# Kernel tuning notes

Hardware: AMD Instinct MI355X
Metric: run time of the kernel (lower is better)

## Reference

```python
import jax, jax.numpy as jnp
import numpy as np

N = 10000       # num_nodes
E = 1000        # num_hyperedges
STEPS = 30      # horizon


def setup_inputs() -> dict:
    key = jax.random.key(0)
    k1, k2 = jax.random.split(key, 2)
    infected0 = jax.random.uniform(k1, (N,)) < 0.01
    x = jnp.stack([(~infected0).astype(jnp.float32),
                   infected0.astype(jnp.float32),
                   jnp.zeros((N,), jnp.float32)], axis=1)
    H = (jax.random.uniform(k2, (STEPS - 1, E, N)) < 0.001).astype(jnp.float32)
    beta = jnp.full((N,), 0.01, jnp.float32)
    gamma = jnp.full((N,), 0.038, jnp.float32)
    return {"x": x, "H": H, "beta": beta, "gamma": gamma, "steps": STEPS}


def _simulate(x, H, beta, gamma):
    n = x.shape[0]
    key0 = jax.random.key(42)

    def step(carry, H_t):
        p_prev, s_prev, key = carry
        key, k1, k2 = jax.random.split(key, 3)
        infected = s_prev[:, 1]
        # hypergraph Laplacian step: H_t.T @ (H_t @ infected)
        new_cases = beta * (H_t.T @ (H_t @ infected))
        new_rec = gamma * infected
        p = jnp.stack([p_prev[:, 0] - new_cases,
                       p_prev[:, 1] + new_cases - new_rec,
                       p_prev[:, 2] + new_rec], axis=1)
        p = jnp.clip(p, 0.0, 1.0)
        # per-node stochastic SIR state transitions (vectorized)
        u1 = jax.random.uniform(k1, (n,))
        u2 = jax.random.uniform(k2, (n,))
        was_S = s_prev[:, 0] == 1
        was_I = s_prev[:, 1] == 1
        s_to_I = was_S & (u1 < p[:, 1])
        i_event = was_I & (u1 < p[:, 2])
        i_to_R = i_event & (u2 < 0.5)
        i_to_S = i_event & ~(u2 < 0.5)
        new_S = (was_S & ~s_to_I) | i_to_S
        new_I = s_to_I | (was_I & ~i_event)
        new_R = (~was_S & ~was_I) | i_to_R
        s = jnp.stack([new_S, new_I, new_R], axis=1).astype(x.dtype)
        return (p, s, key), (p, s)

    (_, _, _), (p_seq, s_seq) = jax.lax.scan(step, (x, x, key0), H)
    pathogen = jnp.concatenate([x[None], p_seq], axis=0)    # (steps, N, 3)
    state = jnp.concatenate([x[None], s_seq], axis=0)       # (steps, N, 3)
    return pathogen, state


def reference(x, H, beta, gamma, steps):
    # steps == H.shape[0] + 1 by construction
    return _simulate(x, H, beta, gamma)
```

## Files before the change

### kernel.cpp

```cpp
#include <hip/hip_runtime.h>
#include <stdint.h>

constexpr int NN = 10000;
constexpr int EE = 1000;
constexpr int TT = 30;
constexpr int TS = TT - 1;
constexpr int ROW = NN * 3;
constexpr int S_OFF = TT * ROW;
constexpr int CAP_E = 48;
constexpr int SIMT = 1024;
constexpr int NPT  = 10;

__host__ __device__ inline void tf2x32(uint32_t k0, uint32_t k1,
                                       uint32_t x0, uint32_t x1,
                                       uint32_t &o0, uint32_t &o1) {
  uint32_t ks2 = k0 ^ k1 ^ 0x1BD11BDAu;
  x0 += k0; x1 += k1;
#define TFR(r) do { x0 += x1; x1 = (x1 << (r)) | (x1 >> (32 - (r))); x1 ^= x0; } while (0)
  TFR(13); TFR(15); TFR(26); TFR(6);
  x0 += k1;  x1 += ks2 + 1u;
  TFR(17); TFR(29); TFR(16); TFR(24);
  x0 += ks2; x1 += k0 + 2u;
  TFR(13); TFR(15); TFR(26); TFR(6);
  x0 += k0;  x1 += k1 + 3u;
  TFR(17); TFR(29); TFR(16); TFR(24);
  x0 += k1;  x1 += ks2 + 4u;
  TFR(13); TFR(15); TFR(26); TFR(6);
  x0 += ks2; x1 += k0 + 5u;
#undef TFR
  o0 = x0; o1 = x1;
}

__device__ inline float bits_to_uniform(uint32_t bits) {
  float f = __uint_as_float((bits >> 9) | 0x3F800000u) - 1.0f;
  return f < 0.f ? 0.f : f;
}

struct StepKeys { uint32_t k1a[TS], k1b[TS], k2a[TS], k2b[TS]; };

__global__ void k_init(const float* __restrict__ x, float* __restrict__ out) {
  int i = blockIdx.x * blockDim.x + threadIdx.x;
  if (i < ROW) { out[i] = x[i]; out[S_OFF + i] = x[i]; }
}

__global__ void k_rand(float* __restrict__ u1, float* __restrict__ u2, StepKeys keys) {
  int t = blockIdx.y;
  int n = blockIdx.x * blockDim.x + threadIdx.x;
  if (n >= NN) return;
  uint32_t a, b;
  tf2x32(keys.k1a[t], keys.k1b[t], 0u, (uint32_t)n, a, b);
  u1[t * NN + n] = bits_to_uniform(a ^ b);
  tf2x32(keys.k2a[t], keys.k2b[t], 0u, (uint32_t)n, a, b);
  u2[t * NN + n] = bits_to_uniform(a ^ b);
}

__global__ void k_scan(const float* __restrict__ H, int* __restrict__ edge_cnt,
                       uint16_t* __restrict__ edge_nodes) {
  const int row = blockIdx.x;
  const int t = row / EE;
  const int e = row - t * EE;
  __shared__ int cnt;
  __shared__ uint16_t list[CAP_E];
  if (threadIdx.x == 0) cnt = 0;
  __syncthreads();
  const float4* hrow = reinterpret_cast<const float4*>(H + (size_t)row * NN);
  for (int i = threadIdx.x; i < NN / 4; i += blockDim.x) {
    float4 v = hrow[i];
    int b4 = i * 4;
    if (v.x != 0.f) { int p = atomicAdd(&cnt, 1); if (p < CAP_E) list[p] = (uint16_t)(b4 + 0); }
    if (v.y != 0.f) { int p = atomicAdd(&cnt, 1); if (p < CAP_E) list[p] = (uint16_t)(b4 + 1); }
    if (v.z != 0.f) { int p = atomicAdd(&cnt, 1); if (p < CAP_E) list[p] = (uint16_t)(b4 + 2); }
    if (v.w != 0.f) { int p = atomicAdd(&cnt, 1); if (p < CAP_E) list[p] = (uint16_t)(b4 + 3); }
  }
  __syncthreads();
  int c = cnt < CAP_E ? cnt : CAP_E;
  if (threadIdx.x == 0) edge_cnt[row] = c;
  if ((int)threadIdx.x < c)
    edge_nodes[((size_t)t * CAP_E + threadIdx.x) * EE + e] = list[threadIdx.x];
}

__global__ __launch_bounds__(SIMT, 4)
void k_sim(float* __restrict__ out, const float* __restrict__ x,
           const int* __restrict__ edge_cnt, const uint16_t* __restrict__ edge_nodes,
           const float* __restrict__ u1, const float* __restrict__ u2,
           const float* __restrict__ beta, const float* __restrict__ gamma_) {
  __shared__ uint8_t s_st[NN];
  __shared__ int nv[NN];
  const int tid = threadIdx.x;

  float p0[NPT], p1[NPT], p2[NPT], bet[NPT], gam[NPT];
#pragma unroll
  for (int k = 0; k < NPT; ++k) {
    int n = tid + k * SIMT;
    if (n < NN) {
      float x0 = x[n * 3 + 0], x1 = x[n * 3 + 1], x2 = x[n * 3 + 2];
      p0[k] = x0; p1[k] = x1; p2[k] = x2;
      s_st[n] = (x1 == 1.f) ? 1 : ((x0 == 1.f) ? 0 : 2);
      bet[k] = beta[n]; gam[k] = gamma_[n];
    }
  }
  __syncthreads();

  for (int t = 0; t < TS; ++t) {
#pragma unroll
    for (int k = 0; k < NPT; ++k) { int n = tid + k * SIMT; if (n < NN) nv[n] = 0; }
    __syncthreads();

    if (tid < EE) {
      int row = t * EE + tid;
      int ec = edge_cnt[row];
      const uint16_t* base = edge_nodes + (size_t)t * CAP_E * EE + tid;
      int s = 0;
      for (int m = 0; m < ec; ++m) s += (s_st[base[(size_t)m * EE]] == 1) ? 1 : 0;
      for (int m = 0; m < ec; ++m) atomicAdd(&nv[base[(size_t)m * EE]], s);
    }
    __syncthreads();

    float* po = out + (size_t)(t + 1) * ROW;
    float* so = out + S_OFF + (size_t)(t + 1) * ROW;
    const float* u1t = u1 + (size_t)t * NN;
    const float* u2t = u2 + (size_t)t * NN;
#pragma unroll
    for (int k = 0; k < NPT; ++k) {
      int n = tid + k * SIMT;
      if (n < NN) {
        int st = s_st[n];
        float s1 = (st == 1) ? 1.f : 0.f;
        float new_cases = __fmul_rn(bet[k], (float)nv[n]);
        float new_rec   = __fmul_rn(gam[k], s1);
        float q0 = fminf(1.f, fmaxf(0.f, __fsub_rn(p0[k], new_cases)));
        float q1 = fminf(1.f, fmaxf(0.f, __fsub_rn(__fadd_rn(p1[k], new_cases), new_rec)));
        float q2 = fminf(1.f, fmaxf(0.f, __fadd_rn(p2[k], new_rec)));
        p0[k] = q0; p1[k] = q1; p2[k] = q2;

        float uu1 = u1t[n], uu2 = u2t[n];
        bool was_S  = (st == 0);
        bool was_I  = (st == 1);
        bool s_to_I = was_S && (uu1 < q1);
        bool i_event = was_I && (uu1 < q2);
        bool u2lt   = (uu2 < 0.5f);
        bool i_to_R = i_event && u2lt;
        bool i_to_S = i_event && !u2lt;
        bool new_S = (was_S && !s_to_I) || i_to_S;
        bool new_I = s_to_I || (was_I && !i_event);
        bool new_R = (!was_S && !was_I) || i_to_R;

        po[n * 3 + 0] = q0; po[n * 3 + 1] = q1; po[n * 3 + 2] = q2;
        so[n * 3 + 0] = new_S ? 1.f : 0.f;
        so[n * 3 + 1] = new_I ? 1.f : 0.f;
        so[n * 3 + 2] = new_R ? 1.f : 0.f;
        s_st[n] = new_I ? 1 : (new_S ? 0 : 2);
      }
    }
    __syncthreads();
  }
}

extern "C" void kernel_launch(void* const* d_in, const int* in_sizes, int n_in,
                              void* d_out, int out_size, void* d_ws, size_t ws_size,
                              hipStream_t stream) {
  const float* x      = (const float*)d_in[0];
  const float* H      = (const float*)d_in[1];
  const float* beta   = (const float*)d_in[2];
  const float* gamma_ = (const float*)d_in[3];
  float* out = (float*)d_out;

  StepKeys keys;
  uint32_t key0 = 0u, key1 = 42u;
  for (int t = 0; t < TS; ++t) {
    uint32_t a0, b0, a1, b1, a2, b2;
    tf2x32(key0, key1, 0u, 0u, a0, b0);
    tf2x32(key0, key1, 0u, 1u, a1, b1);
    tf2x32(key0, key1, 0u, 2u, a2, b2);
    keys.k1a[t] = a1; keys.k1b[t] = b1; keys.k2a[t] = a2; keys.k2b[t] = b2;
    key0 = a0; key1 = b0;
  }

  size_t off = 0;
  auto take = [&](size_t bytes) { size_t o = off; off += (bytes + 255) & ~(size_t)255; return o; };
  size_t o_ec = take((size_t)TS * EE * sizeof(int));
  size_t o_en = take((size_t)TS * EE * CAP_E * sizeof(uint16_t));
  size_t o_u1 = take((size_t)TS * NN * sizeof(float));
  size_t o_u2 = take((size_t)TS * NN * sizeof(float));

  int*      edge_cnt   = (int*)((char*)d_ws + o_ec);
  uint16_t* edge_nodes = (uint16_t*)((char*)d_ws + o_en);
  float*    u1         = (float*)((char*)d_ws + o_u1);
  float*    u2         = (float*)((char*)d_ws + o_u2);

  k_init<<<(ROW + 255) / 256, 256, 0, stream>>>(x, out);
  k_rand<<<dim3((NN + 255) / 256, TS), 256, 0, stream>>>(u1, u2, keys);
  k_scan<<<TS * EE, 256, 0, stream>>>(H, edge_cnt, edge_nodes);
  k_sim<<<1, SIMT, 0, stream>>>(out, x, edge_cnt, edge_nodes, u1, u2, beta, gamma_);
}
```

Before: 1.798 ms.

## Move float output writes out of single-block sim into parallel expand kernel

The single-workgroup simulation kernel now writes only compact per-step uint8 states and uint16 neighbour counts to workspace, instead of six strided floats per node per step. A new grid-wide k_expand kernel replays the cheap probability recurrence from those compact arrays and writes the full pathogen and state outputs in parallel. This moves most of the global-store traffic off the serial one-block critical path, at the cost of an extra launch and recomputation. The uint16 truncation of neighbour counts assumes counts stay below 65536.

```diff
diff --git a/kernel.cpp b/kernel.cpp
--- a/kernel.cpp
+++ b/kernel.cpp
@@ -38,11 +38,6 @@
 
 struct StepKeys { uint32_t k1a[TS], k1b[TS], k2a[TS], k2b[TS]; };
 
-__global__ void k_init(const float* __restrict__ x, float* __restrict__ out) {
-  int i = blockIdx.x * blockDim.x + threadIdx.x;
-  if (i < ROW) { out[i] = x[i]; out[S_OFF + i] = x[i]; }
-}
-
 __global__ void k_rand(float* __restrict__ u1, float* __restrict__ u2, StepKeys keys) {
   int t = blockIdx.y;
   int n = blockIdx.x * blockDim.x + threadIdx.x;
@@ -80,10 +75,11 @@
 }
 
 __global__ __launch_bounds__(SIMT, 4)
-void k_sim(float* __restrict__ out, const float* __restrict__ x,
+void k_sim(const float* __restrict__ x,
            const int* __restrict__ edge_cnt, const uint16_t* __restrict__ edge_nodes,
            const float* __restrict__ u1, const float* __restrict__ u2,
-           const float* __restrict__ beta, const float* __restrict__ gamma_) {
+           const float* __restrict__ beta, const float* __restrict__ gamma_,
+           uint16_t* __restrict__ nvA, uint8_t* __restrict__ stA) {
   __shared__ uint8_t s_st[NN];
   __shared__ int nv[NN];
   const int tid = threadIdx.x;
@@ -93,9 +89,11 @@
   for (int k = 0; k < NPT; ++k) {
     int n = tid + k * SIMT;
     if (n < NN) {
-      float x0 = x[n * 3 + 0], x1 = x[n * 3 + 1], x2 = x[n * 3 + 2];
-      p0[k] = x0; p1[k] = x1; p2[k] = x2;
-      s_st[n] = (x1 == 1.f) ? 1 : ((x0 == 1.f) ? 0 : 2);
+      float x0 = x[n * 3 + 0], x1 = x[n * 3 + 1];
+      p0[k] = x0; p1[k] = x1; p2[k] = x[n * 3 + 2];
+      uint8_t c = (x1 == 1.f) ? 1 : ((x0 == 1.f) ? 0 : 2);
+      s_st[n] = c;
+      stA[n] = c;
       bet[k] = beta[n]; gam[k] = gamma_[n];
     }
   }
@@ -116,17 +114,18 @@
     }
     __syncthreads();
 
-    float* po = out + (size_t)(t + 1) * ROW;
-    float* so = out + S_OFF + (size_t)(t + 1) * ROW;
     const float* u1t = u1 + (size_t)t * NN;
     const float* u2t = u2 + (size_t)t * NN;
+    uint16_t* nvO = nvA + (size_t)t * NN;
+    uint8_t*  stO = stA + (size_t)(t + 1) * NN;
 #pragma unroll
     for (int k = 0; k < NPT; ++k) {
       int n = tid + k * SIMT;
       if (n < NN) {
         int st = s_st[n];
+        int v = nv[n];
         float s1 = (st == 1) ? 1.f : 0.f;
-        float new_cases = __fmul_rn(bet[k], (float)nv[n]);
+        float new_cases = __fmul_rn(bet[k], (float)v);
         float new_rec   = __fmul_rn(gam[k], s1);
         float q0 = fminf(1.f, fmaxf(0.f, __fsub_rn(p0[k], new_cases)));
         float q1 = fminf(1.f, fmaxf(0.f, __fsub_rn(__fadd_rn(p1[k], new_cases), new_rec)));
@@ -139,20 +138,43 @@
         bool s_to_I = was_S && (uu1 < q1);
         bool i_event = was_I && (uu1 < q2);
         bool u2lt   = (uu2 < 0.5f);
-        bool i_to_R = i_event && u2lt;
         bool i_to_S = i_event && !u2lt;
         bool new_S = (was_S && !s_to_I) || i_to_S;
         bool new_I = s_to_I || (was_I && !i_event);
-        bool new_R = (!was_S && !was_I) || i_to_R;
-
-        po[n * 3 + 0] = q0; po[n * 3 + 1] = q1; po[n * 3 + 2] = q2;
-        so[n * 3 + 0] = new_S ? 1.f : 0.f;
-        so[n * 3 + 1] = new_I ? 1.f : 0.f;
-        so[n * 3 + 2] = new_R ? 1.f : 0.f;
-        s_st[n] = new_I ? 1 : (new_S ? 0 : 2);
+        uint8_t c = new_I ? 1 : (new_S ? 0 : 2);
+        s_st[n] = c;
+        stO[n] = c;
+        nvO[n] = (uint16_t)v;
       }
     }
     __syncthreads();
+  }
+}
+
+__global__ void k_expand(float* __restrict__ out, const float* __restrict__ x,
+                         const uint16_t* __restrict__ nvA, const uint8_t* __restrict__ stA,
+                         const float* __restrict__ beta, const float* __restrict__ gamma_) {
+  int n = blockIdx.x * blockDim.x + threadIdx.x;
+  if (n >= NN) return;
+  float p0 = x[n * 3 + 0], p1 = x[n * 3 + 1], p2 = x[n * 3 + 2];
+  float bet = beta[n], gam = gamma_[n];
+  out[n * 3 + 0] = p0; out[n * 3 + 1] = p1; out[n * 3 + 2] = p2;
+  out[S_OFF + n * 3 + 0] = p0; out[S_OFF + n * 3 + 1] = p1; out[S_OFF + n * 3 + 2] = p2;
+  for (int t = 0; t < TS; ++t) {
+    int st = stA[(size_t)t * NN + n];
+    float s1 = (st == 1) ? 1.f : 0.f;
+    float new_cases = __fmul_rn(bet, (float)nvA[(size_t)t * NN + n]);
+    float new_rec   = __fmul_rn(gam, s1);
+    p0 = fminf(1.f, fmaxf(0.f, __fsub_rn(p0, new_cases)));
+    p1 = fminf(1.f, fmaxf(0.f, __fsub_rn(__fadd_rn(p1, new_cases), new_rec)));
+    p2 = fminf(1.f, fmaxf(0.f, __fadd_rn(p2, new_rec)));
+    float* po = out + (size_t)(t + 1) * ROW;
+    float* so = out + S_OFF + (size_t)(t + 1) * ROW;
+    po[n * 3 + 0] = p0; po[n * 3 + 1] = p1; po[n * 3 + 2] = p2;
+    int sn = stA[(size_t)(t + 1) * NN + n];
+    so[n * 3 + 0] = (sn == 0) ? 1.f : 0.f;
+    so[n * 3 + 1] = (sn == 1) ? 1.f : 0.f;
+    so[n * 3 + 2] = (sn == 2) ? 1.f : 0.f;
   }
 }
 
@@ -182,14 +204,18 @@
   size_t o_en = take((size_t)TS * EE * CAP_E * sizeof(uint16_t));
   size_t o_u1 = take((size_t)TS * NN * sizeof(float));
   size_t o_u2 = take((size_t)TS * NN * sizeof(float));
+  size_t o_nv = take((size_t)TS * NN * sizeof(uint16_t));
+  size_t o_st = take((size_t)TT * NN * sizeof(uint8_t));
 
   int*      edge_cnt   = (int*)((char*)d_ws + o_ec);
   uint16_t* edge_nodes = (uint16_t*)((char*)d_ws + o_en);
   float*    u1         = (float*)((char*)d_ws + o_u1);
   float*    u2         = (float*)((char*)d_ws + o_u2);
-
-  k_init<<<(ROW + 255) / 256, 256, 0, stream>>>(x, out);
+  uint16_t* nvA        = (uint16_t*)((char*)d_ws + o_nv);
+  uint8_t*  stA        = (uint8_t*)((char*)d_ws + o_st);
+
   k_rand<<<dim3((NN + 255) / 256, TS), 256, 0, stream>>>(u1, u2, keys);
   k_scan<<<TS * EE, 256, 0, stream>>>(H, edge_cnt, edge_nodes);
-  k_sim<<<1, SIMT, 0, stream>>>(out, x, edge_cnt, edge_nodes, u1, u2, beta, gamma_);
-}
+  k_sim<<<1, SIMT, 0, stream>>>(x, edge_cnt, edge_nodes, u1, u2, beta, gamma_, nvA, stA);
+  k_expand<<<(NN + 255) / 256, 256, 0, stream>>>(out, x, nvA, stA, beta, gamma_);
+}
```

Measured after the change: 1.880 ms. +4.5%, slower.

## Fuse scan and simulation into one kernel with per-step producer/consumer flags

Applied to the files above, without the earlier changes.

Merges the H-row compaction kernel and the single-block simulation kernel into one launch. Block 0 runs the sequential simulation and spins on a per-timestep counter, while the other blocks compact H rows and signal completion with release atomics, so the serial simulation can overlap the bandwidth-bound scan. It also folds the init copy into the sim block, packs edge node indices two per 32-bit word, skips scatter when an edge has no infected nodes, prefetches the random numbers into registers, and drops one barrier per step. The design relies on block 0 being scheduled before the producer blocks and staying resident; otherwise it could deadlock. Scan blocks now use 1024 threads, which may lower scan efficiency.

```diff
diff --git a/kernel.cpp b/kernel.cpp
--- a/kernel.cpp
+++ b/kernel.cpp
@@ -8,6 +8,7 @@
 constexpr int ROW = NN * 3;
 constexpr int S_OFF = TT * ROW;
 constexpr int CAP_E = 48;
+constexpr int WPR = CAP_E / 2;
 constexpr int SIMT = 1024;
 constexpr int NPT  = 10;
 
@@ -38,14 +39,11 @@
 
 struct StepKeys { uint32_t k1a[TS], k1b[TS], k2a[TS], k2b[TS]; };
 
-__global__ void k_init(const float* __restrict__ x, float* __restrict__ out) {
-  int i = blockIdx.x * blockDim.x + threadIdx.x;
-  if (i < ROW) { out[i] = x[i]; out[S_OFF + i] = x[i]; }
-}
-
-__global__ void k_rand(float* __restrict__ u1, float* __restrict__ u2, StepKeys keys) {
+__global__ void k_rand(float* __restrict__ u1, float* __restrict__ u2,
+                       unsigned* __restrict__ cnt, StepKeys keys) {
   int t = blockIdx.y;
   int n = blockIdx.x * blockDim.x + threadIdx.x;
+  if (blockIdx.x == 0 && blockIdx.y == 0 && threadIdx.x < TS) cnt[threadIdx.x] = 0u;
   if (n >= NN) return;
   uint32_t a, b;
   tf2x32(keys.k1a[t], keys.k1b[t], 0u, (uint32_t)n, a, b);
@@ -54,39 +52,50 @@
   u2[t * NN + n] = bits_to_uniform(a ^ b);
 }
 
-__global__ void k_scan(const float* __restrict__ H, int* __restrict__ edge_cnt,
-                       uint16_t* __restrict__ edge_nodes) {
-  const int row = blockIdx.x;
-  const int t = row / EE;
-  const int e = row - t * EE;
-  __shared__ int cnt;
-  __shared__ uint16_t list[CAP_E];
-  if (threadIdx.x == 0) cnt = 0;
-  __syncthreads();
-  const float4* hrow = reinterpret_cast<const float4*>(H + (size_t)row * NN);
-  for (int i = threadIdx.x; i < NN / 4; i += blockDim.x) {
-    float4 v = hrow[i];
-    int b4 = i * 4;
-    if (v.x != 0.f) { int p = atomicAdd(&cnt, 1); if (p < CAP_E) list[p] = (uint16_t)(b4 + 0); }
-    if (v.y != 0.f) { int p = atomicAdd(&cnt, 1); if (p < CAP_E) list[p] = (uint16_t)(b4 + 1); }
-    if (v.z != 0.f) { int p = atomicAdd(&cnt, 1); if (p < CAP_E) list[p] = (uint16_t)(b4 + 2); }
-    if (v.w != 0.f) { int p = atomicAdd(&cnt, 1); if (p < CAP_E) list[p] = (uint16_t)(b4 + 3); }
-  }
-  __syncthreads();
-  int c = cnt < CAP_E ? cnt : CAP_E;
-  if (threadIdx.x == 0) edge_cnt[row] = c;
-  if ((int)threadIdx.x < c)
-    edge_nodes[((size_t)t * CAP_E + threadIdx.x) * EE + e] = list[threadIdx.x];
-}
-
-__global__ __launch_bounds__(SIMT, 4)
-void k_sim(float* __restrict__ out, const float* __restrict__ x,
-           const int* __restrict__ edge_cnt, const uint16_t* __restrict__ edge_nodes,
-           const float* __restrict__ u1, const float* __restrict__ u2,
-           const float* __restrict__ beta, const float* __restrict__ gamma_) {
+__global__ __launch_bounds__(SIMT, 1)
+void k_fused(const float* __restrict__ H,
+             int* __restrict__ edge_cnt, uint32_t* __restrict__ edge_words,
+             unsigned* __restrict__ cnt,
+             const float* __restrict__ x,
+             const float* __restrict__ u1, const float* __restrict__ u2,
+             const float* __restrict__ beta, const float* __restrict__ gamma_,
+             float* __restrict__ out) {
+  const int tid = threadIdx.x;
+
+  if (blockIdx.x > 0) {
+    const int row = blockIdx.x - 1;
+    const int t = row / EE;
+    const int e = row - t * EE;
+    __shared__ int scnt;
+    __shared__ uint16_t list[CAP_E];
+    if (tid == 0) scnt = 0;
+    __syncthreads();
+    const float4* hrow = reinterpret_cast<const float4*>(H + (size_t)row * NN);
+    for (int i = tid; i < NN / 4; i += SIMT) {
+      float4 v = hrow[i];
+      int b4 = i * 4;
+      if (v.x != 0.f) { int p = atomicAdd(&scnt, 1); if (p < CAP_E) list[p] = (uint16_t)(b4 + 0); }
+      if (v.y != 0.f) { int p = atomicAdd(&scnt, 1); if (p < CAP_E) list[p] = (uint16_t)(b4 + 1); }
+      if (v.z != 0.f) { int p = atomicAdd(&scnt, 1); if (p < CAP_E) list[p] = (uint16_t)(b4 + 2); }
+      if (v.w != 0.f) { int p = atomicAdd(&scnt, 1); if (p < CAP_E) list[p] = (uint16_t)(b4 + 3); }
+    }
+    __syncthreads();
+    int c = scnt < CAP_E ? scnt : CAP_E;
+    if (tid == 0) edge_cnt[row] = c;
+    int words = (c + 1) >> 1;
+    if (tid < words) {
+      uint32_t lo = list[2 * tid];
+      uint32_t hi = (2 * tid + 1 < c) ? (uint32_t)list[2 * tid + 1] : 0xFFFFu;
+      edge_words[((size_t)t * WPR + tid) * EE + e] = lo | (hi << 16);
+    }
+    __syncthreads();
+    if (tid == 0)
+      __hip_atomic_fetch_add(&cnt[t], 1u, __ATOMIC_RELEASE, __HIP_MEMORY_SCOPE_AGENT);
+    return;
+  }
+
   __shared__ uint8_t s_st[NN];
   __shared__ int nv[NN];
-  const int tid = threadIdx.x;
 
   float p0[NPT], p1[NPT], p2[NPT], bet[NPT], gam[NPT];
 #pragma unroll
@@ -96,49 +105,77 @@
       float x0 = x[n * 3 + 0], x1 = x[n * 3 + 1], x2 = x[n * 3 + 2];
       p0[k] = x0; p1[k] = x1; p2[k] = x2;
       s_st[n] = (x1 == 1.f) ? 1 : ((x0 == 1.f) ? 0 : 2);
+      nv[n] = 0;
       bet[k] = beta[n]; gam[k] = gamma_[n];
+      out[n * 3 + 0] = x0; out[n * 3 + 1] = x1; out[n * 3 + 2] = x2;
+      out[S_OFF + n * 3 + 0] = x0; out[S_OFF + n * 3 + 1] = x1; out[S_OFF + n * 3 + 2] = x2;
     }
   }
   __syncthreads();
 
   for (int t = 0; t < TS; ++t) {
+    float u1r[NPT], u2r[NPT];
 #pragma unroll
-    for (int k = 0; k < NPT; ++k) { int n = tid + k * SIMT; if (n < NN) nv[n] = 0; }
+    for (int k = 0; k < NPT; ++k) {
+      int n = tid + k * SIMT;
+      if (n < NN) { u1r[k] = u1[(size_t)t * NN + n]; u2r[k] = u2[(size_t)t * NN + n]; }
+    }
+    if (tid == 0) {
+      while (__hip_atomic_load(&cnt[t], __ATOMIC_ACQUIRE, __HIP_MEMORY_SCOPE_AGENT)
+             < (unsigned)EE) {
+        __builtin_amdgcn_s_sleep(16);
+      }
+    }
     __syncthreads();
 
     if (tid < EE) {
-      int row = t * EE + tid;
-      int ec = edge_cnt[row];
-      const uint16_t* base = edge_nodes + (size_t)t * CAP_E * EE + tid;
+      int ec = __hip_atomic_load(&edge_cnt[t * EE + tid], __ATOMIC_RELAXED,
+                                 __HIP_MEMORY_SCOPE_AGENT);
+      if (ec > CAP_E) ec = CAP_E;
+      int words = (ec + 1) >> 1;
+      const uint32_t* wb = edge_words + (size_t)t * WPR * EE + tid;
       int s = 0;
-      for (int m = 0; m < ec; ++m) s += (s_st[base[(size_t)m * EE]] == 1) ? 1 : 0;
-      for (int m = 0; m < ec; ++m) atomicAdd(&nv[base[(size_t)m * EE]], s);
+      for (int mw = 0; mw < words; ++mw) {
+        uint32_t w = __hip_atomic_load(&wb[(size_t)mw * EE], __ATOMIC_RELAXED,
+                                       __HIP_MEMORY_SCOPE_AGENT);
+        s += (s_st[w & 0xFFFFu] == 1) ? 1 : 0;
+        uint32_t hi = w >> 16;
+        if (hi != 0xFFFFu) s += (s_st[hi] == 1) ? 1 : 0;
+      }
+      if (s > 0) {
+        for (int mw = 0; mw < words; ++mw) {
+          uint32_t w = __hip_atomic_load(&wb[(size_t)mw * EE], __ATOMIC_RELAXED,
+                                         __HIP_MEMORY_SCOPE_AGENT);
+          atomicAdd(&nv[w & 0xFFFFu], s);
+          uint32_t hi = w >> 16;
+          if (hi != 0xFFFFu) atomicAdd(&nv[(int)hi], s);
+        }
+      }
     }
     __syncthreads();
 
     float* po = out + (size_t)(t + 1) * ROW;
     float* so = out + S_OFF + (size_t)(t + 1) * ROW;
-    const float* u1t = u1 + (size_t)t * NN;
-    const float* u2t = u2 + (size_t)t * NN;
 #pragma unroll
     for (int k = 0; k < NPT; ++k) {
       int n = tid + k * SIMT;
       if (n < NN) {
         int st = s_st[n];
+        int v = nv[n];
+        nv[n] = 0;
         float s1 = (st == 1) ? 1.f : 0.f;
-        float new_cases = __fmul_rn(bet[k], (float)nv[n]);
+        float new_cases = __fmul_rn(bet[k], (float)v);
         float new_rec   = __fmul_rn(gam[k], s1);
         float q0 = fminf(1.f, fmaxf(0.f, __fsub_rn(p0[k], new_cases)));
         float q1 = fminf(1.f, fmaxf(0.f, __fsub_rn(__fadd_rn(p1[k], new_cases), new_rec)));
         float q2 = fminf(1.f, fmaxf(0.f, __fadd_rn(p2[k], new_rec)));
         p0[k] = q0; p1[k] = q1; p2[k] = q2;
 
-        float uu1 = u1t[n], uu2 = u2t[n];
         bool was_S  = (st == 0);
         bool was_I  = (st == 1);
-        bool s_to_I = was_S && (uu1 < q1);
-        bool i_event = was_I && (uu1 < q2);
-        bool u2lt   = (uu2 < 0.5f);
+        bool s_to_I = was_S && (u1r[k] < q1);
+        bool i_event = was_I && (u1r[k] < q2);
+        bool u2lt   = (u2r[k] < 0.5f);
         bool i_to_R = i_event && u2lt;
         bool i_to_S = i_event && !u2lt;
         bool new_S = (was_S && !s_to_I) || i_to_S;
@@ -152,7 +189,6 @@
         s_st[n] = new_I ? 1 : (new_S ? 0 : 2);
       }
     }
-    __syncthreads();
   }
 }
 
@@ -179,17 +215,18 @@
   size_t off = 0;
   auto take = [&](size_t bytes) { size_t o = off; off += (bytes + 255) & ~(size_t)255; return o; };
   size_t o_ec = take((size_t)TS * EE * sizeof(int));
-  size_t o_en = take((size_t)TS * EE * CAP_E * sizeof(uint16_t));
+  size_t o_ew = take((size_t)TS * WPR * EE * sizeof(uint32_t));
   size_t o_u1 = take((size_t)TS * NN * sizeof(float));
   size_t o_u2 = take((size_t)TS * NN * sizeof(float));
+  size_t o_ct = take((size_t)TS * sizeof(unsigned));
 
   int*      edge_cnt   = (int*)((char*)d_ws + o_ec);
-  uint16_t* edge_nodes = (uint16_t*)((char*)d_ws + o_en);
+  uint32_t* edge_words = (uint32_t*)((char*)d_ws + o_ew);
   float*    u1         = (float*)((char*)d_ws + o_u1);
   float*    u2         = (float*)((char*)d_ws + o_u2);
-
-  k_init<<<(ROW + 255) / 256, 256, 0, stream>>>(x, out);
-  k_rand<<<dim3((NN + 255) / 256, TS), 256, 0, stream>>>(u1, u2, keys);
-  k_scan<<<TS * EE, 256, 0, stream>>>(H, edge_cnt, edge_nodes);
-  k_sim<<<1, SIMT, 0, stream>>>(out, x, edge_cnt, edge_nodes, u1, u2, beta, gamma_);
-}
+  unsigned* cnt        = (unsigned*)((char*)d_ws + o_ct);
+
+  k_rand<<<dim3((NN + 255) / 256, TS), 256, 0, stream>>>(u1, u2, cnt, keys);
+  k_fused<<<1 + TS * EE, SIMT, 0, stream>>>(H, edge_cnt, edge_words, cnt,
+                                            x, u1, u2, beta, gamma_, out);
+}
```

Result: slower. 2.122 ms (+18.0%).

## Pack edge node lists, prefetch, cut barriers and fold init into sim kernel

Applied to the files above, without the earlier changes.

Edge node indices are packed two per 32-bit word with sentinel padding, and the first eight words are prefetched unconditionally so the gather loop is unrolled. The per-step clearing of the count array moves into the update loop, which removes one barrier per step. The remaining barriers become a raw LDS waitcnt plus s_barrier. Random uniforms are loaded before the edge phase, edges with no infected nodes skip their atomics, and the init kernel is merged into the sim kernel. The cost is a more complex scan output layout, and the hand-written barrier relies on no global memory ordering being needed across it.

```diff
diff --git a/kernel.cpp b/kernel.cpp
--- a/kernel.cpp
+++ b/kernel.cpp
@@ -8,6 +8,8 @@
 constexpr int ROW = NN * 3;
 constexpr int S_OFF = TT * ROW;
 constexpr int CAP_E = 48;
+constexpr int WPR = CAP_E / 2;
+constexpr int PREW = 8;
 constexpr int SIMT = 1024;
 constexpr int NPT  = 10;
 
@@ -38,9 +40,8 @@
 
 struct StepKeys { uint32_t k1a[TS], k1b[TS], k2a[TS], k2b[TS]; };
 
-__global__ void k_init(const float* __restrict__ x, float* __restrict__ out) {
-  int i = blockIdx.x * blockDim.x + threadIdx.x;
-  if (i < ROW) { out[i] = x[i]; out[S_OFF + i] = x[i]; }
+__device__ inline void bar_lds() {
+  asm volatile("s_waitcnt lgkmcnt(0)\n\ts_barrier" ::: "memory");
 }
 
 __global__ void k_rand(float* __restrict__ u1, float* __restrict__ u2, StepKeys keys) {
@@ -55,7 +56,7 @@
 }
 
 __global__ void k_scan(const float* __restrict__ H, int* __restrict__ edge_cnt,
-                       uint16_t* __restrict__ edge_nodes) {
+                       uint32_t* __restrict__ edge_words) {
   const int row = blockIdx.x;
   const int t = row / EE;
   const int e = row - t * EE;
@@ -75,13 +76,19 @@
   __syncthreads();
   int c = cnt < CAP_E ? cnt : CAP_E;
   if (threadIdx.x == 0) edge_cnt[row] = c;
-  if ((int)threadIdx.x < c)
-    edge_nodes[((size_t)t * CAP_E + threadIdx.x) * EE + e] = list[threadIdx.x];
+  int words = (c + 1) >> 1;
+  int wmax = words > PREW ? words : PREW;
+  if ((int)threadIdx.x < wmax) {
+    int j = threadIdx.x;
+    uint32_t lo = (2 * j     < c) ? (uint32_t)list[2 * j]     : 0xFFFFu;
+    uint32_t hi = (2 * j + 1 < c) ? (uint32_t)list[2 * j + 1] : 0xFFFFu;
+    edge_words[((size_t)t * WPR + j) * EE + e] = lo | (hi << 16);
+  }
 }
 
 __global__ __launch_bounds__(SIMT, 4)
 void k_sim(float* __restrict__ out, const float* __restrict__ x,
-           const int* __restrict__ edge_cnt, const uint16_t* __restrict__ edge_nodes,
+           const int* __restrict__ edge_cnt, const uint32_t* __restrict__ edge_words,
            const float* __restrict__ u1, const float* __restrict__ u2,
            const float* __restrict__ beta, const float* __restrict__ gamma_) {
   __shared__ uint8_t s_st[NN];
@@ -96,49 +103,81 @@
       float x0 = x[n * 3 + 0], x1 = x[n * 3 + 1], x2 = x[n * 3 + 2];
       p0[k] = x0; p1[k] = x1; p2[k] = x2;
       s_st[n] = (x1 == 1.f) ? 1 : ((x0 == 1.f) ? 0 : 2);
+      nv[n] = 0;
       bet[k] = beta[n]; gam[k] = gamma_[n];
-    }
-  }
-  __syncthreads();
+      out[n * 3 + 0] = x0; out[n * 3 + 1] = x1; out[n * 3 + 2] = x2;
+      out[S_OFF + n * 3 + 0] = x0; out[S_OFF + n * 3 + 1] = x1; out[S_OFF + n * 3 + 2] = x2;
+    }
+  }
+  bar_lds();
 
   for (int t = 0; t < TS; ++t) {
-#pragma unroll
-    for (int k = 0; k < NPT; ++k) { int n = tid + k * SIMT; if (n < NN) nv[n] = 0; }
-    __syncthreads();
+    float u1r[NPT], u2r[NPT];
+#pragma unroll
+    for (int k = 0; k < NPT; ++k) {
+      int n = tid + k * SIMT;
+      if (n < NN) { u1r[k] = u1[(size_t)t * NN + n]; u2r[k] = u2[(size_t)t * NN + n]; }
+    }
 
     if (tid < EE) {
-      int row = t * EE + tid;
-      int ec = edge_cnt[row];
-      const uint16_t* base = edge_nodes + (size_t)t * CAP_E * EE + tid;
+      const uint32_t* wb = edge_words + (size_t)t * WPR * EE + tid;
+      int ec = edge_cnt[t * EE + tid]; if (ec > CAP_E) ec = CAP_E;
+      uint32_t w[PREW];
+#pragma unroll
+      for (int j = 0; j < PREW; ++j) w[j] = wb[(size_t)j * EE];
+      int words = (ec + 1) >> 1;
       int s = 0;
-      for (int m = 0; m < ec; ++m) s += (s_st[base[(size_t)m * EE]] == 1) ? 1 : 0;
-      for (int m = 0; m < ec; ++m) atomicAdd(&nv[base[(size_t)m * EE]], s);
-    }
-    __syncthreads();
+#pragma unroll
+      for (int j = 0; j < PREW; ++j) {
+        uint32_t lo = w[j] & 0xFFFFu, hi = w[j] >> 16;
+        if (lo != 0xFFFFu) s += (s_st[lo] == 1) ? 1 : 0;
+        if (hi != 0xFFFFu) s += (s_st[hi] == 1) ? 1 : 0;
+      }
+      for (int j = PREW; j < words; ++j) {
+        uint32_t ww = wb[(size_t)j * EE];
+        uint32_t lo = ww & 0xFFFFu, hi = ww >> 16;
+        if (lo != 0xFFFFu) s += (s_st[lo] == 1) ? 1 : 0;
+        if (hi != 0xFFFFu) s += (s_st[hi] == 1) ? 1 : 0;
+      }
+      if (s > 0) {
+#pragma unroll
+        for (int j = 0; j < PREW; ++j) {
+          uint32_t lo = w[j] & 0xFFFFu, hi = w[j] >> 16;
+          if (lo != 0xFFFFu) atomicAdd(&nv[lo], s);
+          if (hi != 0xFFFFu) atomicAdd(&nv[hi], s);
+        }
+        for (int j = PREW; j < words; ++j) {
+          uint32_t ww = wb[(size_t)j * EE];
+          uint32_t lo = ww & 0xFFFFu, hi = ww >> 16;
+          if (lo != 0xFFFFu) atomicAdd(&nv[lo], s);
+          if (hi != 0xFFFFu) atomicAdd(&nv[hi], s);
+        }
+      }
+    }
+    bar_lds();
 
     float* po = out + (size_t)(t + 1) * ROW;
     float* so = out + S_OFF + (size_t)(t + 1) * ROW;
-    const float* u1t = u1 + (size_t)t * NN;
-    const float* u2t = u2 + (size_t)t * NN;
 #pragma unroll
     for (int k = 0; k < NPT; ++k) {
       int n = tid + k * SIMT;
       if (n < NN) {
         int st = s_st[n];
+        int v = nv[n];
+        nv[n] = 0;
         float s1 = (st == 1) ? 1.f : 0.f;
-        float new_cases = __fmul_rn(bet[k], (float)nv[n]);
+        float new_cases = __fmul_rn(bet[k], (float)v);
         float new_rec   = __fmul_rn(gam[k], s1);
         float q0 = fminf(1.f, fmaxf(0.f, __fsub_rn(p0[k], new_cases)));
         float q1 = fminf(1.f, fmaxf(0.f, __fsub_rn(__fadd_rn(p1[k], new_cases), new_rec)));
         float q2 = fminf(1.f, fmaxf(0.f, __fadd_rn(p2[k], new_rec)));
         p0[k] = q0; p1[k] = q1; p2[k] = q2;
 
-        float uu1 = u1t[n], uu2 = u2t[n];
         bool was_S  = (st == 0);
         bool was_I  = (st == 1);
-        bool s_to_I = was_S && (uu1 < q1);
-        bool i_event = was_I && (uu1 < q2);
-        bool u2lt   = (uu2 < 0.5f);
+        bool s_to_I = was_S && (u1r[k] < q1);
+        bool i_event = was_I && (u1r[k] < q2);
+        bool u2lt   = (u2r[k] < 0.5f);
         bool i_to_R = i_event && u2lt;
         bool i_to_S = i_event && !u2lt;
         bool new_S = (was_S && !s_to_I) || i_to_S;
@@ -152,7 +191,7 @@
         s_st[n] = new_I ? 1 : (new_S ? 0 : 2);
       }
     }
-    __syncthreads();
+    bar_lds();
   }
 }
 
@@ -179,17 +218,16 @@
   size_t off = 0;
   auto take = [&](size_t bytes) { size_t o = off; off += (bytes + 255) & ~(size_t)255; return o; };
   size_t o_ec = take((size_t)TS * EE * sizeof(int));
-  size_t o_en = take((size_t)TS * EE * CAP_E * sizeof(uint16_t));
+  size_t o_ew = take((size_t)TS * WPR * EE * sizeof(uint32_t));
   size_t o_u1 = take((size_t)TS * NN * sizeof(float));
   size_t o_u2 = take((size_t)TS * NN * sizeof(float));
 
   int*      edge_cnt   = (int*)((char*)d_ws + o_ec);
-  uint16_t* edge_nodes = (uint16_t*)((char*)d_ws + o_en);
+  uint32_t* edge_words = (uint32_t*)((char*)d_ws + o_ew);
   float*    u1         = (float*)((char*)d_ws + o_u1);
   float*    u2         = (float*)((char*)d_ws + o_u2);
 
-  k_init<<<(ROW + 255) / 256, 256, 0, stream>>>(x, out);
   k_rand<<<dim3((NN + 255) / 256, TS), 256, 0, stream>>>(u1, u2, keys);
-  k_scan<<<TS * EE, 256, 0, stream>>>(H, edge_cnt, edge_nodes);
-  k_sim<<<1, SIMT, 0, stream>>>(out, x, edge_cnt, edge_nodes, u1, u2, beta, gamma_);
-}
+  k_scan<<<TS * EE, 256, 0, stream>>>(H, edge_cnt, edge_words);
+  k_sim<<<1, SIMT, 0, stream>>>(out, x, edge_cnt, edge_words, u1, u2, beta, gamma_);
+}
```

Measured after the change: 1.754 ms. 2.5% less time.
